# Performance work log

Hardware: AMD Instinct MI355X
Metric: run time of the kernel (lower is better)

The kernel has to match this reference:

```python
import jax, jax.numpy as jnp
import numpy as np

_EPS = 1e-6

def _qmul(q1, q2):  # xyzw quaternion product
    x1, y1, z1, w1 = q1[..., 0], q1[..., 1], q1[..., 2], q1[..., 3]
    x2, y2, z2, w2 = q2[..., 0], q2[..., 1], q2[..., 2], q2[..., 3]
    return jnp.stack([
        w1 * x2 + x1 * w2 + y1 * z2 - z1 * y2,
        w1 * y2 + y1 * w2 + z1 * x2 - x1 * z2,
        w1 * z2 + z1 * w2 + x1 * y2 - y1 * x2,
        w1 * w2 - x1 * x2 - y1 * y2 - z1 * z2], axis=-1)

def _qrot(q, v):  # rotate v by unit quaternion q (xyzw)
    qv, qw = q[..., :3], q[..., 3:4]
    t = 2.0 * jnp.cross(qv, v)
    return v + qw * t + jnp.cross(qv, t)

def _so3_log(q):  # quaternion (xyzw) -> rotation vector phi
    qv, qw = q[..., :3], q[..., 3:4]
    n2 = jnp.sum(qv * qv, axis=-1, keepdims=True)
    small = n2 < _EPS * _EPS
    n = jnp.sqrt(jnp.where(small, 1.0, n2))
    factor = jnp.where(small,
                       2.0 / qw - (2.0 / 3.0) * n2 / qw ** 3,
                       2.0 * jnp.arctan2(n, qw) / n)
    return factor * qv

def _so3_exp(phi):  # rotation vector -> quaternion (xyzw)
    t2 = jnp.sum(phi * phi, axis=-1, keepdims=True)
    small = t2 < _EPS * _EPS
    theta = jnp.sqrt(jnp.where(small, 1.0, t2))
    half = 0.5 * theta
    s = jnp.where(small, 0.5 - t2 / 48.0, jnp.sin(half) / theta)
    w = jnp.where(small, 1.0 - t2 / 8.0, jnp.cos(half))
    return jnp.concatenate([s * phi, w], axis=-1)

def _jl(phi, v):  # SO3 left Jacobian J_l(phi) @ v
    t2 = jnp.sum(phi * phi, axis=-1, keepdims=True)
    small = t2 < _EPS * _EPS
    t2s = jnp.where(small, 1.0, t2)
    theta = jnp.sqrt(t2s)
    a = jnp.where(small, 0.5 - t2 / 24.0, (1.0 - jnp.cos(theta)) / t2s)
    b = jnp.where(small, 1.0 / 6.0 - t2 / 120.0, (theta - jnp.sin(theta)) / (t2s * theta))
    c1 = jnp.cross(phi, v)
    return v + a * c1 + b * jnp.cross(phi, c1)

def _jl_inv(phi, v):  # SO3 left Jacobian inverse J_l^{-1}(phi) @ v
    t2 = jnp.sum(phi * phi, axis=-1, keepdims=True)
    small = t2 < _EPS * _EPS
    t2s = jnp.where(small, 1.0, t2)
    theta = jnp.sqrt(t2s)
    s = jnp.sin(theta)
    s_safe = jnp.where(jnp.abs(s) < _EPS, _EPS, s)
    c = jnp.where(small, 1.0 / 12.0 + t2 / 720.0,
                  1.0 / t2s - (1.0 + jnp.cos(theta)) / (2.0 * theta * s_safe))
    c1 = jnp.cross(phi, v)
    return v - 0.5 * c1 + c * jnp.cross(phi, c1)

def _se3_inv(T):
    t, q = T[..., :3], T[..., 3:]
    qi = q * jnp.array([-1.0, -1.0, -1.0, 1.0], dtype=T.dtype)
    return jnp.concatenate([-_qrot(qi, t), qi], axis=-1)

def _se3_mul(T1, T2):
    t1, q1 = T1[..., :3], T1[..., 3:]
    t2, q2 = T2[..., :3], T2[..., 3:]
    return jnp.concatenate([t1 + _qrot(q1, t2), _qmul(q1, q2)], axis=-1)

def _se3_log(T):  # SE3 -> se3 [tau, phi]
    t, q = T[..., :3], T[..., 3:]
    phi = _so3_log(q)
    return jnp.concatenate([_jl_inv(phi, t), phi], axis=-1)

def _se3_exp(xi):  # se3 [tau, phi] -> SE3
    tau, phi = xi[..., :3], xi[..., 3:]
    q = _so3_exp(phi)
    return jnp.concatenate([_jl(phi, tau), q], axis=-1)

def _forward(input_poses, time):
    # duplicate first/last pose (inter_begin_and_end=True)
    poses = jnp.concatenate([input_poses[:, :1], input_poses, input_poses[:, -1:]], axis=1)
    B, P = poses.shape[0], poses.shape[1]
    S = P - 3  # number of spline segments
    u = time.reshape(-1)  # [K]
    K = u.shape[0]
    U = jnp.stack([jnp.ones_like(u), u, u * u, u * u * u], axis=0)  # [4,K]
    M = jnp.array([[5., 3., -3., 1.], [1., 3., 3., -2.], [0., 0., 0., 1.]], dtype=u.dtype) / 6.0
    w = M @ U  # [3,K] cumulative B-spline weights
    p0, p1 = poses[:, 0:S], poses[:, 1:S + 1]
    p2, p3 = poses[:, 2:S + 2], poses[:, 3:S + 3]
    d0 = _se3_log(_se3_mul(_se3_inv(p0), p1))  # [B,S,6]
    d1 = _se3_log(_se3_mul(_se3_inv(p1), p2))
    d2 = _se3_log(_se3_mul(_se3_inv(p2), p3))
    A0 = _se3_exp(d0[:, :, None, :] * w[0][None, None, :, None])  # [B,S,K,7]
    A1 = _se3_exp(d1[:, :, None, :] * w[1][None, None, :, None])
    A2 = _se3_exp(d2[:, :, None, :] * w[2][None, None, :, None])
    Td = jnp.broadcast_to(p0[:, :, None, :], (B, S, K, 7))
    out = _se3_mul(_se3_mul(_se3_mul(Td, A0), A1), A2)
    return out.reshape(B, S * K, 7)

def setup_inputs() -> dict:
    key = jax.random.key(0)
    k1, k2, k3 = jax.random.split(key, 3)
    B, N, K = 32, 2048, 32
    t = jax.random.normal(k1, (B, N, 3), dtype=jnp.float32) * 2.0
    q = jax.random.normal(k2, (B, N, 4), dtype=jnp.float32)
    q = q / jnp.linalg.norm(q, axis=-1, keepdims=True)
    q = jnp.where(q[..., 3:4] < 0, -q, q)  # qw >= 0 for well-conditioned Log
    input_poses = jnp.concatenate([t, q], axis=-1)
    time = jax.random.uniform(k3, (1, 1, K), dtype=jnp.float32)
    return {"input_poses": input_poses, "time": time}

def reference(input_poses, time):
    return _forward(input_poses, time)
```

## Files before the change

kernel.cpp:

```cpp
#include <hip/hip_runtime.h>
#include <cmath>

namespace {

constexpr int BATCH = 32;
constexpr int NPOSE = 2048;
constexpr int KSAMP = 32;
constexpr int NSEG  = NPOSE - 1;
constexpr int SEGB  = 8;
constexpr float EPS  = 1e-6f;
constexpr float EPS2 = 1e-12f;
constexpr float INV_TWO_PI = 0.15915494309189535f;

struct V3 { float x, y, z; };
struct Q4 { float x, y, z, w; };
struct SE3 { V3 t; Q4 q; };

__device__ __forceinline__ float frcp(float x)  { return __builtin_amdgcn_rcpf(x); }
__device__ __forceinline__ float fsqrt(float x) { return __builtin_amdgcn_sqrtf(x); }
__device__ __forceinline__ float fsin(float x)  { return __builtin_amdgcn_sinf(x * INV_TWO_PI); }
__device__ __forceinline__ float fcos(float x)  { return __builtin_amdgcn_cosf(x * INV_TWO_PI); }

__device__ __forceinline__ V3 v3add(V3 a, V3 b) { return {a.x + b.x, a.y + b.y, a.z + b.z}; }
__device__ __forceinline__ V3 v3sub(V3 a, V3 b) { return {a.x - b.x, a.y - b.y, a.z - b.z}; }
__device__ __forceinline__ V3 v3scl(V3 a, float s) { return {a.x * s, a.y * s, a.z * s}; }
__device__ __forceinline__ float v3dot(V3 a, V3 b) { return a.x * b.x + a.y * b.y + a.z * b.z; }
__device__ __forceinline__ V3 v3cross(V3 a, V3 b) {
    return {a.y * b.z - a.z * b.y, a.z * b.x - a.x * b.z, a.x * b.y - a.y * b.x};
}

__device__ __forceinline__ V3 qrot(Q4 q, V3 v) {
    V3 qv{q.x, q.y, q.z};
    V3 t = v3scl(v3cross(qv, v), 2.0f);
    return v3add(v3add(v, v3scl(t, q.w)), v3cross(qv, t));
}

__device__ __forceinline__ Q4 qmul(Q4 a, Q4 b) {
    return {a.w * b.x + a.x * b.w + a.y * b.z - a.z * b.y,
            a.w * b.y + a.y * b.w + a.z * b.x - a.x * b.z,
            a.w * b.z + a.z * b.w + a.x * b.y - a.y * b.x,
            a.w * b.w - a.x * b.x - a.y * b.y - a.z * b.z};
}

__device__ __forceinline__ V3 so3_log(Q4 q) {
    V3 qv{q.x, q.y, q.z};
    float n2 = v3dot(qv, qv);
    bool small = n2 < EPS2;
    float n = fsqrt(small ? 1.0f : n2);
    float iw = frcp(q.w);
    float f_small = 2.0f * iw - (2.0f / 3.0f) * n2 * iw * iw * iw;
    float f_big = 2.0f * atan2f(n, q.w) * frcp(n);
    float factor = small ? f_small : f_big;
    return v3scl(qv, factor);
}

__device__ __forceinline__ V3 jl_inv(V3 phi, V3 v) {
    float t2 = v3dot(phi, phi);
    bool small = t2 < EPS2;
    float t2s = small ? 1.0f : t2;
    float theta = fsqrt(t2s);
    float s = fsin(theta), cth = fcos(theta);
    float s_safe = (fabsf(s) < EPS) ? EPS : s;
    float c_big = frcp(t2s) - (1.0f + cth) * frcp(2.0f * theta * s_safe);
    float c = small ? (1.0f / 12.0f + t2 * (1.0f / 720.0f)) : c_big;
    V3 c1 = v3cross(phi, v);
    return v3add(v3sub(v, v3scl(c1, 0.5f)), v3scl(v3cross(phi, c1), c));
}

__device__ __forceinline__ SE3 se3_exp(V3 tau, V3 phi) {
    float t2 = v3dot(phi, phi);
    bool small = t2 < EPS2;
    float t2s = small ? 1.0f : t2;
    float inv_t2s = frcp(t2s);
    float theta = fsqrt(t2s);
    float inv_theta = frcp(theta);
    float half = 0.5f * theta;
    float sh = fsin(half), ch = fcos(half);
    float sin_t = 2.0f * sh * ch;
    float s  = small ? (0.5f - t2 * (1.0f / 48.0f))  : sh * inv_theta;
    float qw = small ? (1.0f - t2 * (1.0f / 8.0f))   : ch;
    float a  = small ? (0.5f - t2 * (1.0f / 24.0f))  : 2.0f * sh * sh * inv_t2s;
    float bb = small ? (1.0f / 6.0f - t2 * (1.0f / 120.0f))
                     : (theta - sin_t) * inv_t2s * inv_theta;
    SE3 r;
    r.q = {s * phi.x, s * phi.y, s * phi.z, qw};
    V3 c1 = v3cross(phi, tau);
    r.t = v3add(v3add(tau, v3scl(c1, a)), v3scl(v3cross(phi, c1), bb));
    return r;
}

__device__ __forceinline__ SE3 se3_mul(SE3 A, SE3 Bv) {
    SE3 r;
    r.t = v3add(A.t, qrot(A.q, Bv.t));
    r.q = qmul(A.q, Bv.q);
    return r;
}

__global__ __launch_bounds__(256) void lie_spline_kernel(
    const float* __restrict__ poses,
    const float* __restrict__ timev,
    float* __restrict__ out)
{
    __shared__ float sd[SEGB + 2][6];
    __shared__ float sw[3 * KSAMP];
    __shared__ float sp[SEGB * 7];
    __shared__ __align__(16) float stage[SEGB * KSAMP * 7];

    const int b   = blockIdx.y;
    const int s0  = blockIdx.x * SEGB;
    const int tid = threadIdx.x;

    if (tid < SEGB + 2) {
        int i = s0 + tid;
        if (i <= NPOSE) {
            int ia = max(i - 1, 0);
            int ib = min(i, NPOSE - 1);
            const float* Pa = poses + ((size_t)b * NPOSE + ia) * 7;
            const float* Pb = poses + ((size_t)b * NPOSE + ib) * 7;
            V3 ta{Pa[0], Pa[1], Pa[2]}; Q4 qa{Pa[3], Pa[4], Pa[5], Pa[6]};
            V3 tb{Pb[0], Pb[1], Pb[2]}; Q4 qb{Pb[3], Pb[4], Pb[5], Pb[6]};
            Q4 qi{-qa.x, -qa.y, -qa.z, qa.w};
            V3 trel = qrot(qi, v3sub(tb, ta));
            Q4 qrel = qmul(qi, qb);
            V3 phi = so3_log(qrel);
            V3 tau = jl_inv(phi, trel);
            sd[tid][0] = tau.x; sd[tid][1] = tau.y; sd[tid][2] = tau.z;
            sd[tid][3] = phi.x; sd[tid][4] = phi.y; sd[tid][5] = phi.z;
        }
    } else if (tid >= 64 && tid < 64 + KSAMP) {
        int l = tid - 64;
        float u = timev[l];
        float u2 = u * u, u3 = u2 * u;
        const float c6 = 1.0f / 6.0f;
        sw[l]             = (5.0f + 3.0f * u - 3.0f * u2 + u3) * c6;
        sw[KSAMP + l]     = (1.0f + 3.0f * u + 3.0f * u2 - 2.0f * u3) * c6;
        sw[2 * KSAMP + l] = u3 * c6;
    } else if (tid >= 128 && tid < 128 + SEGB * 7) {
        int j = tid - 128;
        int jseg = j / 7, jf = j - jseg * 7;
        int ip = max(s0 + jseg - 1, 0);
        sp[j] = poses[((size_t)b * NPOSE + ip) * 7 + jf];
    }
    __syncthreads();

    const int lane = tid & (KSAMP - 1);
    const int seg  = tid >> 5;
    const int s    = s0 + seg;

    if (s < NSEG) {
        float w0 = sw[lane], w1 = sw[KSAMP + lane], w2 = sw[2 * KSAMP + lane];

        V3 d0t{sd[seg][0],     sd[seg][1],     sd[seg][2]};
        V3 d0p{sd[seg][3],     sd[seg][4],     sd[seg][5]};
        V3 d1t{sd[seg + 1][0], sd[seg + 1][1], sd[seg + 1][2]};
        V3 d1p{sd[seg + 1][3], sd[seg + 1][4], sd[seg + 1][5]};
        V3 d2t{sd[seg + 2][0], sd[seg + 2][1], sd[seg + 2][2]};
        V3 d2p{sd[seg + 2][3], sd[seg + 2][4], sd[seg + 2][5]};

        const float* P0 = sp + seg * 7;
        SE3 T{{P0[0], P0[1], P0[2]}, {P0[3], P0[4], P0[5], P0[6]}};

        T = se3_mul(T, se3_exp(v3scl(d0t, w0), v3scl(d0p, w0)));
        T = se3_mul(T, se3_exp(v3scl(d1t, w1), v3scl(d1p, w1)));
        T = se3_mul(T, se3_exp(v3scl(d2t, w2), v3scl(d2p, w2)));

        float* st = stage + (size_t)tid * 7;
        st[0] = T.t.x; st[1] = T.t.y; st[2] = T.t.z;
        st[3] = T.q.x; st[4] = T.q.y; st[5] = T.q.z; st[6] = T.q.w;
    }
    __syncthreads();

    int nseg_blk = min(NSEG - s0, SEGB);
    int nvec = nseg_blk * (KSAMP * 7 / 4);
    const float4* sv = reinterpret_cast<const float4*>(stage);
    float4* ov = reinterpret_cast<float4*>(out + ((size_t)b * NSEG + s0) * (size_t)(KSAMP * 7));
    for (int j = tid; j < nvec; j += 256) ov[j] = sv[j];
}

}

extern "C" void kernel_launch(void* const* d_in, const int* in_sizes, int n_in,
                              void* d_out, int out_size, void* d_ws, size_t ws_size,
                              hipStream_t stream) {
    const float* poses = (const float*)d_in[0];
    const float* timev = (const float*)d_in[1];
    float* out = (float*)d_out;
    (void)in_sizes; (void)n_in; (void)out_size; (void)d_ws; (void)ws_size;

    dim3 grid((NSEG + SEGB - 1) / SEGB, BATCH);
    lie_spline_kernel<<<grid, 256, 0, stream>>>(poses, timev, out);
}
```

Measured before the change: 92.56 us.

## Precompute per-delta axis/cross terms in a separate kernel and simplify SE3 exp

Splits the work into two kernels. The first computes each SE3 log delta once and stores its norm, unit axis and the cross products of axis with tau in a workspace. The second kernel evaluates the spline exp in closed form from those precomputed terms, which drops per-sample cross products, small-angle branches and shared-memory weight tables, and it replaces atan2 with a polynomial acos. This removes the delta work that neighbouring blocks repeated and shortens the per-sample ALU path, in exchange for a second launch, a workspace round trip and a possible loss of accuracy from the acos approximation and the clamped small-angle handling.

After: 89.67 us. 1.03x faster.

```diff
diff --git a/kernel.cpp b/kernel.cpp
--- a/kernel.cpp
+++ b/kernel.cpp
@@ -3,11 +3,12 @@
 
 namespace {
 
-constexpr int BATCH = 32;
-constexpr int NPOSE = 2048;
-constexpr int KSAMP = 32;
-constexpr int NSEG  = NPOSE - 1;
-constexpr int SEGB  = 8;
+constexpr int BATCH  = 32;
+constexpr int NPOSE  = 2048;
+constexpr int KSAMP  = 32;
+constexpr int NSEG   = NPOSE - 1;
+constexpr int NDELTA = NPOSE + 1;
+constexpr int SEGB   = 8;
 constexpr float EPS  = 1e-6f;
 constexpr float EPS2 = 1e-12f;
 constexpr float INV_TWO_PI = 0.15915494309189535f;
@@ -40,6 +41,27 @@
             a.w * b.y + a.y * b.w + a.z * b.x - a.x * b.z,
             a.w * b.z + a.z * b.w + a.x * b.y - a.y * b.x,
             a.w * b.w - a.x * b.x - a.y * b.y - a.z * b.z};
+}
+
+__device__ __forceinline__ SE3 se3_mul(SE3 A, SE3 Bv) {
+    SE3 r;
+    r.t = v3add(A.t, qrot(A.q, Bv.t));
+    r.q = qmul(A.q, Bv.q);
+    return r;
+}
+
+__device__ __forceinline__ float facos(float x) {
+    float ax = fabsf(x);
+    float p = -0.0012624911f;
+    p = p * ax + 0.0066700901f;
+    p = p * ax - 0.0170881256f;
+    p = p * ax + 0.0308918810f;
+    p = p * ax - 0.0501743046f;
+    p = p * ax + 0.0889789874f;
+    p = p * ax - 0.2145988016f;
+    p = p * ax + 1.5707963050f;
+    float r = fsqrt(fmaxf(1.0f - ax, 0.0f)) * p;
+    return (x >= 0.0f) ? r : (3.14159265358979f - r);
 }
 
 __device__ __forceinline__ V3 so3_log(Q4 q) {
@@ -49,9 +71,9 @@
     float n = fsqrt(small ? 1.0f : n2);
     float iw = frcp(q.w);
     float f_small = 2.0f * iw - (2.0f / 3.0f) * n2 * iw * iw * iw;
-    float f_big = 2.0f * atan2f(n, q.w) * frcp(n);
-    float factor = small ? f_small : f_big;
-    return v3scl(qv, factor);
+    float wc = fminf(fmaxf(q.w, -1.0f), 1.0f);
+    float f_big = 2.0f * facos(wc) * frcp(n);
+    return v3scl(qv, small ? f_small : f_big);
 }
 
 __device__ __forceinline__ V3 jl_inv(V3 phi, V3 v) {
@@ -67,79 +89,79 @@
     return v3add(v3sub(v, v3scl(c1, 0.5f)), v3scl(v3cross(phi, c1), c));
 }
 
-__device__ __forceinline__ SE3 se3_exp(V3 tau, V3 phi) {
-    float t2 = v3dot(phi, phi);
-    bool small = t2 < EPS2;
-    float t2s = small ? 1.0f : t2;
-    float inv_t2s = frcp(t2s);
-    float theta = fsqrt(t2s);
-    float inv_theta = frcp(theta);
-    float half = 0.5f * theta;
-    float sh = fsin(half), ch = fcos(half);
-    float sin_t = 2.0f * sh * ch;
-    float s  = small ? (0.5f - t2 * (1.0f / 48.0f))  : sh * inv_theta;
-    float qw = small ? (1.0f - t2 * (1.0f / 8.0f))   : ch;
-    float a  = small ? (0.5f - t2 * (1.0f / 24.0f))  : 2.0f * sh * sh * inv_t2s;
-    float bb = small ? (1.0f / 6.0f - t2 * (1.0f / 120.0f))
-                     : (theta - sin_t) * inv_t2s * inv_theta;
+__global__ __launch_bounds__(256) void lie_delta_kernel(
+    const float* __restrict__ poses,
+    float4* __restrict__ ws)
+{
+    const int i = blockIdx.x * 256 + threadIdx.x;
+    const int b = blockIdx.y;
+    if (i >= NDELTA) return;
+
+    int ia = max(i - 1, 0);
+    int ib = min(i, NPOSE - 1);
+    const float* Pa = poses + ((size_t)b * NPOSE + ia) * 7;
+    const float* Pb = poses + ((size_t)b * NPOSE + ib) * 7;
+    V3 ta{Pa[0], Pa[1], Pa[2]}; Q4 qa{Pa[3], Pa[4], Pa[5], Pa[6]};
+    V3 tb{Pb[0], Pb[1], Pb[2]}; Q4 qb{Pb[3], Pb[4], Pb[5], Pb[6]};
+
+    Q4 qi{-qa.x, -qa.y, -qa.z, qa.w};
+    V3 trel = qrot(qi, v3sub(tb, ta));
+    Q4 qrel = qmul(qi, qb);
+    V3 phi = so3_log(qrel);
+    V3 tau = jl_inv(phi, trel);
+
+    float n2 = v3dot(phi, phi);
+    float nphi = fsqrt(n2);
+    float inv_n = frcp(fmaxf(nphi, 1e-20f));
+    V3 u  = v3scl(phi, inv_n);
+    V3 c1 = v3cross(u, tau);
+    V3 c2 = v3cross(u, c1);
+
+    float4* row = ws + ((size_t)b * NDELTA + i) * 4;
+    row[0] = make_float4(tau.x, tau.y, tau.z, nphi);
+    row[1] = make_float4(u.x,  u.y,  u.z,  0.0f);
+    row[2] = make_float4(c1.x, c1.y, c1.z, 0.0f);
+    row[3] = make_float4(c2.x, c2.y, c2.z, 0.0f);
+}
+
+__device__ __forceinline__ SE3 exp_fast(float4 A, float4 U, float4 C1, float4 C2, float w) {
+    float th = fmaxf(w * A.w, 1e-12f);
+    float sh = fsin(0.5f * th), ch = fcos(0.5f * th);
+    float it = frcp(th);
+    float sA = 2.0f * sh * sh * it;
+    float sB = 1.0f - 2.0f * sh * ch * it;
     SE3 r;
-    r.q = {s * phi.x, s * phi.y, s * phi.z, qw};
-    V3 c1 = v3cross(phi, tau);
-    r.t = v3add(v3add(tau, v3scl(c1, a)), v3scl(v3cross(phi, c1), bb));
-    return r;
-}
-
-__device__ __forceinline__ SE3 se3_mul(SE3 A, SE3 Bv) {
-    SE3 r;
-    r.t = v3add(A.t, qrot(A.q, Bv.t));
-    r.q = qmul(A.q, Bv.q);
+    r.q = {sh * U.x, sh * U.y, sh * U.z, ch};
+    r.t = {w * (A.x + sA * C1.x + sB * C2.x),
+           w * (A.y + sA * C1.y + sB * C2.y),
+           w * (A.z + sA * C1.z + sB * C2.z)};
     return r;
 }
 
 __global__ __launch_bounds__(256) void lie_spline_kernel(
     const float* __restrict__ poses,
     const float* __restrict__ timev,
+    const float4* __restrict__ ws,
     float* __restrict__ out)
 {
-    __shared__ float sd[SEGB + 2][6];
-    __shared__ float sw[3 * KSAMP];
-    __shared__ float sp[SEGB * 7];
+    __shared__ float4 sdel[(SEGB + 2) * 4];
+    __shared__ float  sp[SEGB * 8];
     __shared__ __align__(16) float stage[SEGB * KSAMP * 7];
 
     const int b   = blockIdx.y;
     const int s0  = blockIdx.x * SEGB;
     const int tid = threadIdx.x;
 
-    if (tid < SEGB + 2) {
-        int i = s0 + tid;
-        if (i <= NPOSE) {
-            int ia = max(i - 1, 0);
-            int ib = min(i, NPOSE - 1);
-            const float* Pa = poses + ((size_t)b * NPOSE + ia) * 7;
-            const float* Pb = poses + ((size_t)b * NPOSE + ib) * 7;
-            V3 ta{Pa[0], Pa[1], Pa[2]}; Q4 qa{Pa[3], Pa[4], Pa[5], Pa[6]};
-            V3 tb{Pb[0], Pb[1], Pb[2]}; Q4 qb{Pb[3], Pb[4], Pb[5], Pb[6]};
-            Q4 qi{-qa.x, -qa.y, -qa.z, qa.w};
-            V3 trel = qrot(qi, v3sub(tb, ta));
-            Q4 qrel = qmul(qi, qb);
-            V3 phi = so3_log(qrel);
-            V3 tau = jl_inv(phi, trel);
-            sd[tid][0] = tau.x; sd[tid][1] = tau.y; sd[tid][2] = tau.z;
-            sd[tid][3] = phi.x; sd[tid][4] = phi.y; sd[tid][5] = phi.z;
+    {
+        int nrow4 = min(SEGB + 2, NDELTA - s0) * 4;
+        if (tid < nrow4)
+            sdel[tid] = ws[((size_t)b * NDELTA + s0) * 4 + tid];
+        else if (tid >= 64 && tid < 64 + SEGB * 7) {
+            int j = tid - 64;
+            int jseg = j / 7, jf = j - jseg * 7;
+            int ip = max(s0 + jseg - 1, 0);
+            sp[jseg * 8 + jf] = poses[((size_t)b * NPOSE + ip) * 7 + jf];
         }
-    } else if (tid >= 64 && tid < 64 + KSAMP) {
-        int l = tid - 64;
-        float u = timev[l];
-        float u2 = u * u, u3 = u2 * u;
-        const float c6 = 1.0f / 6.0f;
-        sw[l]             = (5.0f + 3.0f * u - 3.0f * u2 + u3) * c6;
-        sw[KSAMP + l]     = (1.0f + 3.0f * u + 3.0f * u2 - 2.0f * u3) * c6;
-        sw[2 * KSAMP + l] = u3 * c6;
-    } else if (tid >= 128 && tid < 128 + SEGB * 7) {
-        int j = tid - 128;
-        int jseg = j / 7, jf = j - jseg * 7;
-        int ip = max(s0 + jseg - 1, 0);
-        sp[j] = poses[((size_t)b * NPOSE + ip) * 7 + jf];
     }
     __syncthreads();
 
@@ -148,21 +170,20 @@
     const int s    = s0 + seg;
 
     if (s < NSEG) {
-        float w0 = sw[lane], w1 = sw[KSAMP + lane], w2 = sw[2 * KSAMP + lane];
-
-        V3 d0t{sd[seg][0],     sd[seg][1],     sd[seg][2]};
-        V3 d0p{sd[seg][3],     sd[seg][4],     sd[seg][5]};
-        V3 d1t{sd[seg + 1][0], sd[seg + 1][1], sd[seg + 1][2]};
-        V3 d1p{sd[seg + 1][3], sd[seg + 1][4], sd[seg + 1][5]};
-        V3 d2t{sd[seg + 2][0], sd[seg + 2][1], sd[seg + 2][2]};
-        V3 d2p{sd[seg + 2][3], sd[seg + 2][4], sd[seg + 2][5]};
-
-        const float* P0 = sp + seg * 7;
+        float u  = timev[lane];
+        float u2 = u * u, u3 = u2 * u;
+        const float c6 = 1.0f / 6.0f;
+        float w0 = (5.0f + 3.0f * u - 3.0f * u2 + u3) * c6;
+        float w1 = (1.0f + 3.0f * u + 3.0f * u2 - 2.0f * u3) * c6;
+        float w2 = u3 * c6;
+
+        const float* P0 = sp + seg * 8;
         SE3 T{{P0[0], P0[1], P0[2]}, {P0[3], P0[4], P0[5], P0[6]}};
 
-        T = se3_mul(T, se3_exp(v3scl(d0t, w0), v3scl(d0p, w0)));
-        T = se3_mul(T, se3_exp(v3scl(d1t, w1), v3scl(d1p, w1)));
-        T = se3_mul(T, se3_exp(v3scl(d2t, w2), v3scl(d2p, w2)));
+        const float4* r0 = sdel + seg * 4;
+        T = se3_mul(T, exp_fast(r0[0], r0[1], r0[2],  r0[3],  w0));
+        T = se3_mul(T, exp_fast(r0[4], r0[5], r0[6],  r0[7],  w1));
+        T = se3_mul(T, exp_fast(r0[8], r0[9], r0[10], r0[11], w2));
 
         float* st = stage + (size_t)tid * 7;
         st[0] = T.t.x; st[1] = T.t.y; st[2] = T.t.z;
@@ -185,8 +206,12 @@
     const float* poses = (const float*)d_in[0];
     const float* timev = (const float*)d_in[1];
     float* out = (float*)d_out;
-    (void)in_sizes; (void)n_in; (void)out_size; (void)d_ws; (void)ws_size;
-
-    dim3 grid((NSEG + SEGB - 1) / SEGB, BATCH);
-    lie_spline_kernel<<<grid, 256, 0, stream>>>(poses, timev, out);
-}
+    float4* ws = (float4*)d_ws;
+    (void)in_sizes; (void)n_in; (void)out_size; (void)ws_size;
+
+    dim3 g1((NDELTA + 255) / 256, BATCH);
+    lie_delta_kernel<<<g1, 256, 0, stream>>>(poses, ws);
+
+    dim3 g2((NSEG + SEGB - 1) / SEGB, BATCH);
+    lie_spline_kernel<<<g2, 256, 0, stream>>>(poses, timev, ws, out);
+}
```
